# Performance work log

Hardware: AMD Instinct MI355X
Metric: run time of the kernel (lower is better)

## Reference

```python
import jax, jax.numpy as jnp
import numpy as np
from jax import lax

VOL, PATCH, DIM, DEPTH, HEADS, DIM_HEAD, MLP, CH, B = 64, 8, 768, 4, 12, 64, 3072, 1, 2
INNER = HEADS * DIM_HEAD
GS = VOL // PATCH              # 8 -> N = 512 tokens
EPS = 1e-5


def _sincos_1d(embed_dim, pos):
    omega = np.arange(embed_dim // 2, dtype=float) / (embed_dim / 2.0)
    omega = 1.0 / 10000 ** omega
    out = np.einsum('m,d->md', pos.reshape(-1), omega)
    return np.concatenate([np.sin(out), np.cos(out)], axis=1)


def _pos_embed_3d(embed_dim, gs):
    gd = np.arange(gs, dtype=np.float32)
    gh = np.arange(gs, dtype=np.float32)
    gw = np.arange(gs, dtype=np.float32)
    grid = np.stack(np.meshgrid(gw, gh, gd), axis=0).reshape([3, 1, gs, gs, gs])
    emb = np.concatenate([_sincos_1d(embed_dim // 3, grid[i]) for i in range(3)], axis=1)
    return jnp.asarray(emb, jnp.float32)[None]  # [1, N, dim]


def setup_inputs() -> dict:
    key = jax.random.key(0)
    ks = jax.random.split(key, 12)
    s = 0.02  # xavier-like small init scale
    d = {
        'volume': jax.random.normal(ks[0], (B, CH, VOL, VOL, VOL), jnp.float32),
        'conv_w': jax.random.normal(ks[1], (DIM, CH, PATCH, PATCH, PATCH), jnp.float32) * s,
        'conv_b': jnp.zeros((DIM,), jnp.float32),
        'pos_embed': _pos_embed_3d(DIM, GS),
        'ln1_w': jnp.ones((DEPTH, DIM), jnp.float32),
        'ln1_b': jnp.zeros((DEPTH, DIM), jnp.float32),
        'w_qkv': jax.random.normal(ks[2], (DEPTH, DIM, 3 * INNER), jnp.float32) * s,
        'w_o': jax.random.normal(ks[3], (DEPTH, INNER, DIM), jnp.float32) * s,
        'b_o': jnp.zeros((DEPTH, DIM), jnp.float32),
        'ln2_w': jnp.ones((DEPTH, DIM), jnp.float32),
        'ln2_b': jnp.zeros((DEPTH, DIM), jnp.float32),
        'w1': jax.random.normal(ks[4], (DEPTH, DIM, MLP), jnp.float32) * s,
        'b1': jnp.zeros((DEPTH, MLP), jnp.float32),
        'w2': jax.random.normal(ks[5], (DEPTH, MLP, DIM), jnp.float32) * s,
        'b2': jnp.zeros((DEPTH, DIM), jnp.float32),
        'lnf_w': jnp.ones((DIM,), jnp.float32),
        'lnf_b': jnp.zeros((DIM,), jnp.float32),
    }
    return d


def _ln(x, w, b):
    m = jnp.mean(x, axis=-1, keepdims=True)
    v = jnp.mean(jnp.square(x - m), axis=-1, keepdims=True)
    return (x - m) * lax.rsqrt(v + EPS) * w + b


def _forward(volume, conv_w, conv_b, pos_embed, ln1_w, ln1_b, w_qkv, w_o, b_o,
             ln2_w, ln2_b, w1, b1, w2, b2, lnf_w, lnf_b):
    # Conv3d patch embedding (stride == kernel == patch)
    x = lax.conv_general_dilated(volume, conv_w, window_strides=(PATCH,) * 3,
                                 padding='VALID',
                                 dimension_numbers=('NCDHW', 'OIDHW', 'NCDHW'))
    x = x + conv_b[None, :, None, None, None]
    b = x.shape[0]
    x = x.reshape(b, DIM, -1).transpose(0, 2, 1)   # b (d h w) c -> [B, N, dim]
    x = x + pos_embed
    scale = DIM_HEAD ** -0.5

    def layer(x, p):
        l1w, l1b, wqkv, wo, bo, l2w, l2b, W1, B1, W2, B2 = p
        h = _ln(x, l1w, l1b)
        qkv = h @ wqkv                               # [B, N, 3*inner]
        q, k, v = jnp.split(qkv, 3, axis=-1)
        def heads(t):
            bsz, n, _ = t.shape
            return t.reshape(bsz, n, HEADS, DIM_HEAD).transpose(0, 2, 1, 3)
        q, k, v = heads(q), heads(k), heads(v)
        attn = jax.nn.softmax(jnp.einsum('bhqd,bhkd->bhqk', q, k) * scale, axis=-1)
        o = jnp.einsum('bhqk,bhkd->bhqd', attn, v)   # [B, H, N, dh]
        o = o.transpose(0, 2, 1, 3).reshape(x.shape[0], -1, INNER)
        x = x + (o @ wo + bo)
        h = _ln(x, l2w, l2b)
        x = x + (jnp.tanh(h @ W1 + B1) @ W2 + B2)
        return x, None

    params = (ln1_w, ln1_b, w_qkv, w_o, b_o, ln2_w, ln2_b, w1, b1, w2, b2)
    x, _ = lax.scan(layer, x, params)
    return _ln(x, lnf_w, lnf_b)


def reference(volume, conv_w, conv_b, pos_embed, ln1_w, ln1_b, w_qkv, w_o, b_o,
              ln2_w, ln2_b, w1, b1, w2, b2, lnf_w, lnf_b):
    return _forward(volume, conv_w, conv_b, pos_embed, ln1_w, ln1_b, w_qkv, w_o, b_o,
                    ln2_w, ln2_b, w1, b1, w2, b2, lnf_w, lnf_b)
```

## Files before the change

### kernel.cpp

```cpp
#include <hip/hip_runtime.h>
#include <hip/hip_bf16.h>

typedef __hip_bfloat16 bf16;
typedef short bf16x8 __attribute__((ext_vector_type(8)));
typedef float f32x4 __attribute__((ext_vector_type(4)));

__device__ __forceinline__ float b2f(bf16 v) { return __bfloat162float(v); }
__device__ __forceinline__ void storev(float* p, float v) { *p = v; }
__device__ __forceinline__ void storev(bf16* p, float v) { *p = __float2bfloat16(v); }

__device__ __forceinline__ void store4(float* p, float a, float b, float c, float d) {
  *(float4*)p = make_float4(a, b, c, d);
}
__device__ __forceinline__ void store4(bf16* p, float a, float b, float c, float d) {
  bf16 pk[4] = {__float2bfloat16(a), __float2bfloat16(b), __float2bfloat16(c),
                __float2bfloat16(d)};
  *(uint2*)p = *(uint2*)pk;
}

__device__ __forceinline__ void gl2lds16(const bf16* g, bf16* l) {
  __builtin_amdgcn_global_load_lds(
      (const __attribute__((address_space(1))) unsigned int*)g,
      (__attribute__((address_space(3))) unsigned int*)l, 16, 0, 0);
}
__device__ __forceinline__ void gl2lds16f(const float* g, float* l) {
  __builtin_amdgcn_global_load_lds(
      (const __attribute__((address_space(1))) unsigned int*)g,
      (__attribute__((address_space(3))) unsigned int*)l, 16, 0, 0);
}

__global__ __launch_bounds__(256) void prologue_all(
    const float* __restrict__ wqkv, const float* __restrict__ wo,
    const float* __restrict__ w1, const float* __restrict__ w2,
    bf16* __restrict__ tqkv, bf16* __restrict__ two,
    bf16* __restrict__ t1, bf16* __restrict__ t2,
    const float* __restrict__ convw, bf16* __restrict__ cwb,
    const float* __restrict__ vol, bf16* __restrict__ patchA) {
  int bid = blockIdx.x;
  size_t L = blockIdx.y;
  int tid = threadIdx.x;

  if (bid >= 864) {
    if (bid < 960) {
      int cid = (bid - 864) * 4 + (int)L;
      int i = (cid * 256 + tid) * 4;
      float4 v = *(const float4*)&convw[i];
      bf16 pk[4] = {__float2bfloat16(v.x), __float2bfloat16(v.y),
                    __float2bfloat16(v.z), __float2bfloat16(v.w)};
      *(uint2*)&cwb[i] = *(uint2*)pk;
    } else {
      int t = (bid - 960) * 4 + (int)L;
      int b = t >> 9, n = t & 511;
      int pd = n >> 6, ph = (n >> 3) & 7, pw = n & 7;
      const float* vb = vol + ((size_t)b << 18);
      for (int l = tid; l < 512; l += 256) {
        int i = l >> 6, j = (l >> 3) & 7, k = l & 7;
        patchA[(size_t)t * 512 + l] =
            __float2bfloat16(vb[(pd * 8 + i) * 4096 + (ph * 8 + j) * 64 + (pw * 8 + k)]);
      }
    }
    return;
  }

  const float* in;
  bf16* out;
  int R, C, tc, t0;
  if (bid < 216)       { in = wqkv + L * 768 * 2304; out = tqkv + L * 768 * 2304; R = 768;  C = 2304; tc = 36; t0 = bid; }
  else if (bid < 288)  { in = wo + L * 768 * 768;    out = two + L * 768 * 768;   R = 768;  C = 768;  tc = 12; t0 = bid - 216; }
  else if (bid < 576)  { in = w1 + L * 768 * 3072;   out = t1 + L * 768 * 3072;   R = 768;  C = 3072; tc = 48; t0 = bid - 288; }
  else                 { in = w2 + L * 3072 * 768;   out = t2 + L * 3072 * 768;   R = 3072; C = 768;  tc = 12; t0 = bid - 576; }
  int r0 = (t0 / tc) * 128, c0 = (t0 % tc) * 64;
  __shared__ float tile[8192];
#pragma unroll
  for (int it = 0; it < 8; ++it) {
    int s = tid + it * 256;
    int r = s >> 4, cc = s & 15;
    int csrc = (cc ^ ((r >> 3) & 7)) << 2;
    gl2lds16f(&in[(size_t)(r0 + r) * C + c0 + csrc], &tile[s * 4]);
  }
  __syncthreads();
#pragma unroll
  for (int it = 0; it < 4; ++it) {
    int idx = tid + it * 256;
    int c = idx >> 4, rb = (idx & 15) * 8;
    int slot = (c >> 2) ^ ((rb >> 3) & 7);
    int base = rb * 64 + slot * 4 + (c & 3);
    bf16 pk[8];
#pragma unroll
    for (int e = 0; e < 8; ++e) pk[e] = __float2bfloat16(tile[base + e * 64]);
    *(uint4*)&out[(size_t)(c0 + c) * R + r0 + rb] = *(uint4*)pk;
  }
}

template <typename OutT>
__global__ __launch_bounds__(256) void ln_kernel(const float* __restrict__ x,
                                                 const float* __restrict__ w,
                                                 const float* __restrict__ b,
                                                 OutT* __restrict__ out) {
  int row = (blockIdx.x << 2) + (threadIdx.x >> 6);
  int lane = threadIdx.x & 63;
  const float* xr = x + (size_t)row * 768;
  float4 v[3];
  float s = 0.f, ss = 0.f;
#pragma unroll
  for (int j = 0; j < 3; ++j) {
    v[j] = *(const float4*)&xr[j * 256 + lane * 4];
    s += v[j].x + v[j].y + v[j].z + v[j].w;
    ss += v[j].x * v[j].x + v[j].y * v[j].y + v[j].z * v[j].z + v[j].w * v[j].w;
  }
#pragma unroll
  for (int off = 32; off; off >>= 1) {
    s += __shfl_xor(s, off);
    ss += __shfl_xor(ss, off);
  }
  float m = s * (1.f / 768.f);
  float r = rsqrtf(ss * (1.f / 768.f) - m * m + 1e-5f);
  OutT* orow = out + (size_t)row * 768;
#pragma unroll
  for (int j = 0; j < 3; ++j) {
    int cidx = j * 256 + lane * 4;
    float4 wv = *(const float4*)&w[cidx];
    float4 bv = *(const float4*)&b[cidx];
    store4(orow + cidx,
           (v[j].x - m) * r * wv.x + bv.x,
           (v[j].y - m) * r * wv.y + bv.y,
           (v[j].z - m) * r * wv.z + bv.z,
           (v[j].w - m) * r * wv.w + bv.w);
  }
}

template <int BM, int BN, int WR, int WC, int EPI>
__global__ __launch_bounds__(256) void mfma_gemm(
    const bf16* __restrict__ A, const bf16* __restrict__ Bt,
    const float* __restrict__ bias, const float* __restrict__ aux,
    bf16* __restrict__ vt,
    void* __restrict__ Cout, int M, int N, int K) {
  constexpr int WTM = BM / WR, WTN = BN / WC;
  constexpr int MT = WTM / 16, NT = WTN / 16;
  __shared__ bf16 As[BM * 64];
  __shared__ bf16 Bs[BN * 64];
  int tid = threadIdx.x;
  int wave = tid >> 6, lane = tid & 63;
  int wm = wave / WC, wn = wave % WC;
  int m15 = lane & 15, q = lane >> 4;
  int m0 = blockIdx.y * BM, n0 = blockIdx.x * BN;
  int kspan = K / gridDim.z;
  int kbeg = blockIdx.z * kspan, kend = kbeg + kspan;

  f32x4 acc[MT][NT];
#pragma unroll
  for (int i = 0; i < MT; ++i)
#pragma unroll
    for (int j = 0; j < NT; ++j) acc[i][j] = (f32x4){0.f, 0.f, 0.f, 0.f};

  for (int k0 = kbeg; k0 < kend; k0 += 64) {
#pragma unroll
    for (int it = 0; it < BM * 8 / 256; ++it) {
      int c = tid + it * 256;
      int row = c >> 3, cc = c & 7;
      gl2lds16(&A[(size_t)(m0 + row) * K + k0 + cc * 8], &As[c * 8]);
    }
#pragma unroll
    for (int it = 0; it < BN * 8 / 256; ++it) {
      int c = tid + it * 256;
      int row = c >> 3, cc = c & 7;
      gl2lds16(&Bt[(size_t)(n0 + row) * K + k0 + cc * 8], &Bs[c * 8]);
    }
    __syncthreads();
#pragma unroll
    for (int s = 0; s < 2; ++s) {
      bf16x8 af[MT], bfr[NT];
#pragma unroll
      for (int i = 0; i < MT; ++i)
        af[i] = *(const bf16x8*)&As[(wm * WTM + i * 16 + m15) * 64 + s * 32 + q * 8];
#pragma unroll
      for (int j = 0; j < NT; ++j)
        bfr[j] = *(const bf16x8*)&Bs[(wn * WTN + j * 16 + m15) * 64 + s * 32 + q * 8];
#pragma unroll
      for (int i = 0; i < MT; ++i)
#pragma unroll
        for (int j = 0; j < NT; ++j)
          acc[i][j] = __builtin_amdgcn_mfma_f32_16x16x32_bf16(af[i], bfr[j], acc[i][j], 0, 0, 0);
    }
    __syncthreads();
  }

#pragma unroll
  for (int i = 0; i < MT; ++i) {
#pragma unroll
    for (int j = 0; j < NT; ++j) {
      int col = n0 + wn * WTN + j * 16 + m15;
      if (EPI == 4) {
        if (col < 1536) {
#pragma unroll
          for (int r = 0; r < 4; ++r) {
            int row = m0 + wm * WTM + i * 16 + q * 4 + r;
            ((bf16*)Cout)[(size_t)row * 1536 + col] = __float2bfloat16(acc[i][j][r]);
          }
        } else {
          int row0 = m0 + wm * WTM + i * 16 + q * 4;
          int cl = col - 1536;
          int hh = cl >> 6, dd = cl & 63;
          int bb = row0 >> 9, tok = row0 & 511;
          bf16 pk[4];
#pragma unroll
          for (int r = 0; r < 4; ++r) pk[r] = __float2bfloat16(acc[i][j][r]);
          *(uint2*)&vt[((size_t)(bb * 12 + hh) * 64 + dd) * 512 + tok] = *(uint2*)pk;
        }
      } else if (EPI == 5) {
        float bv = (blockIdx.z == 0) ? bias[col] : 0.f;
#pragma unroll
        for (int r = 0; r < 4; ++r) {
          int row = m0 + wm * WTM + i * 16 + q * 4 + r;
          unsafeAtomicAdd(&((float*)Cout)[(size_t)row * N + col], acc[i][j][r] + bv);
        }
      } else {
        float bv = (EPI == 0) ? 0.f : bias[col];
#pragma unroll
        for (int r = 0; r < 4; ++r) {
          int row = m0 + wm * WTM + i * 16 + q * 4 + r;
          float v = acc[i][j][r] + bv;
          if (EPI == 2) v = tanhf(v);
          if (EPI == 3) v += aux[(size_t)(row & 511) * N + col];
          if (EPI == 0 || EPI == 2)
            ((bf16*)Cout)[(size_t)row * N + col] = __float2bfloat16(v);
          else
            ((float*)Cout)[(size_t)row * N + col] = v;
        }
      }
    }
  }
}

__global__ __launch_bounds__(128) void attn_mfma(const bf16* __restrict__ qk,
                                                 const bf16* __restrict__ Vt,
                                                 bf16* __restrict__ o) {
  constexpr int PS = 520;
  __shared__ bf16 KVs[2][64 * 64];
  __shared__ bf16 P[32 * PS];
  int bh = blockIdx.x;
  int b = bh / 12, hh = bh % 12;
  int q0 = blockIdx.y * 32;
  int tid = threadIdx.x;
  int wave = tid >> 6, lane = tid & 63;
  int n15 = lane & 15, quad = lane >> 4;
  const bf16* qkb = qk + (size_t)b * 512 * 1536;
  int ql = wave * 16 + n15;

  const bf16* qp = qkb + (size_t)(q0 + ql) * 1536 + hh * 64 + quad * 8;
  bf16x8 qf0 = *(const bf16x8*)qp;
  bf16x8 qf1 = *(const bf16x8*)(qp + 32);

  f32x4 S[32];
#pragma unroll
  for (int i = 0; i < 32; ++i) S[i] = (f32x4){0.f, 0.f, 0.f, 0.f};

  const bf16* kbase = qkb + 768 + hh * 64;
#pragma unroll
  for (int kr = 0; kr < 4; ++kr) {
    __syncthreads();
#pragma unroll
    for (int h = 0; h < 2; ++h) {
      int kc = kr * 2 + h;
#pragma unroll
      for (int it = 0; it < 4; ++it) {
        int c = tid + it * 128;
        int r = c >> 3, cc = c & 7;
        gl2lds16(&kbase[(size_t)(kc * 64 + r) * 1536 + cc * 8], &KVs[h][c * 8]);
      }
    }
    __syncthreads();
#pragma unroll
    for (int h = 0; h < 2; ++h) {
      int kc = kr * 2 + h;
#pragma unroll
      for (int t = 0; t < 4; ++t) {
        int idx = kc * 4 + t;
        bf16x8 a0 = *(const bf16x8*)&KVs[h][(t * 16 + n15) * 64 + quad * 8];
        bf16x8 a1 = *(const bf16x8*)&KVs[h][(t * 16 + n15) * 64 + 32 + quad * 8];
        S[idx] = __builtin_amdgcn_mfma_f32_16x16x32_bf16(a0, qf0, S[idx], 0, 0, 0);
        S[idx] = __builtin_amdgcn_mfma_f32_16x16x32_bf16(a1, qf1, S[idx], 0, 0, 0);
      }
    }
  }

  float mx = -1e30f;
#pragma unroll
  for (int i = 0; i < 32; ++i)
#pragma unroll
    for (int r = 0; r < 4; ++r) { S[i][r] *= 0.125f; mx = fmaxf(mx, S[i][r]); }
  mx = fmaxf(mx, __shfl_xor(mx, 16));
  mx = fmaxf(mx, __shfl_xor(mx, 32));
  float sum = 0.f;
#pragma unroll
  for (int i = 0; i < 32; ++i)
#pragma unroll
    for (int r = 0; r < 4; ++r) { float e = __expf(S[i][r] - mx); S[i][r] = e; sum += e; }
  sum += __shfl_xor(sum, 16);
  sum += __shfl_xor(sum, 32);
  float inv = 1.f / sum;

#pragma unroll
  for (int i = 0; i < 32; ++i) {
    bf16 pk[4];
#pragma unroll
    for (int r = 0; r < 4; ++r) pk[r] = __float2bfloat16(S[i][r] * inv);
    *(uint2*)&P[(size_t)ql * PS + i * 16 + quad * 4] = *(uint2*)pk;
  }

  f32x4 oacc[4];
#pragma unroll
  for (int dt = 0; dt < 4; ++dt) oacc[dt] = (f32x4){0.f, 0.f, 0.f, 0.f};
  const bf16* vtb = Vt + (size_t)bh * 64 * 512;
#pragma unroll
  for (int kr = 0; kr < 4; ++kr) {
    __syncthreads();
#pragma unroll
    for (int h = 0; h < 2; ++h) {
      int kv = kr * 2 + h;
#pragma unroll
      for (int it = 0; it < 4; ++it) {
        int c = tid + it * 128;
        int r = c >> 3, cc = c & 7;
        gl2lds16(&vtb[(size_t)r * 512 + kv * 64 + cc * 8], &KVs[h][c * 8]);
      }
    }
    __syncthreads();
#pragma unroll
    for (int h = 0; h < 2; ++h) {
      int kv = kr * 2 + h;
      bf16x8 p0 = *(const bf16x8*)&P[(size_t)ql * PS + kv * 64 + quad * 8];
      bf16x8 p1 = *(const bf16x8*)&P[(size_t)ql * PS + kv * 64 + 32 + quad * 8];
#pragma unroll
      for (int dt = 0; dt < 4; ++dt) {
        bf16x8 v0 = *(const bf16x8*)&KVs[h][(dt * 16 + n15) * 64 + quad * 8];
        bf16x8 v1 = *(const bf16x8*)&KVs[h][(dt * 16 + n15) * 64 + 32 + quad * 8];
        oacc[dt] = __builtin_amdgcn_mfma_f32_16x16x32_bf16(p0, v0, oacc[dt], 0, 0, 0);
        oacc[dt] = __builtin_amdgcn_mfma_f32_16x16x32_bf16(p1, v1, oacc[dt], 0, 0, 0);
      }
    }
  }

#pragma unroll
  for (int dt = 0; dt < 4; ++dt)
#pragma unroll
    for (int r = 0; r < 4; ++r) {
      int tok = q0 + wave * 16 + quad * 4 + r;
      o[((size_t)b * 512 + tok) * 768 + hh * 64 + dt * 16 + n15] =
          __float2bfloat16(oacc[dt][r]);
    }
}

extern "C" void kernel_launch(void* const* d_in, const int* in_sizes, int n_in,
                              void* d_out, int out_size, void* d_ws, size_t ws_size,
                              hipStream_t stream) {
  const float* volume = (const float*)d_in[0];
  const float* conv_w = (const float*)d_in[1];
  const float* conv_b = (const float*)d_in[2];
  const float* pos    = (const float*)d_in[3];
  const float* ln1w   = (const float*)d_in[4];
  const float* ln1b   = (const float*)d_in[5];
  const float* wqkv   = (const float*)d_in[6];
  const float* wo     = (const float*)d_in[7];
  const float* bo     = (const float*)d_in[8];
  const float* ln2w   = (const float*)d_in[9];
  const float* ln2b   = (const float*)d_in[10];
  const float* w1     = (const float*)d_in[11];
  const float* b1     = (const float*)d_in[12];
  const float* w2     = (const float*)d_in[13];
  const float* b2     = (const float*)d_in[14];
  const float* lnfw   = (const float*)d_in[15];
  const float* lnfb   = (const float*)d_in[16];

  char* w = (char*)d_ws;
  float* x    = (float*)(w + 0);
  bf16* h     = (bf16*)(w + 3145728);
  bf16* qk    = (bf16*)(w + 4718592);
  bf16* patchA= qk;
  bf16* Vt    = (bf16*)(w + 7864320);
  bf16* oact  = (bf16*)(w + 9437184);
  bf16* cwb   = (bf16*)(w + 15728640);
  bf16* tqkv  = (bf16*)(w + 16515072);
  bf16* two   = (bf16*)(w + 30670848);
  bf16* t1    = (bf16*)(w + 35389440);
  bf16* t2    = (bf16*)(w + 54263808);

  prologue_all<<<dim3(1216, 4), 256, 0, stream>>>(
      wqkv, wo, w1, w2, tqkv, two, t1, t2, conv_w, cwb, volume, patchA);
  mfma_gemm<64, 64, 2, 2, 3><<<dim3(12, 16), 256, 0, stream>>>(
      patchA, cwb, conv_b, pos, nullptr, x, 1024, 768, 512);

  for (int L = 0; L < 4; ++L) {
    ln_kernel<bf16><<<256, 256, 0, stream>>>(x, ln1w + L * 768, ln1b + L * 768, h);
    mfma_gemm<64, 64, 2, 2, 4><<<dim3(36, 16), 256, 0, stream>>>(
        h, tqkv + (size_t)L * 768 * 2304, nullptr, nullptr, Vt, qk, 1024, 2304, 768);
    attn_mfma<<<dim3(24, 16), 128, 0, stream>>>(qk, Vt, oact);
    mfma_gemm<64, 64, 2, 2, 5><<<dim3(12, 16, 2), 256, 0, stream>>>(
        oact, two + (size_t)L * 768 * 768, bo + L * 768, nullptr, nullptr, x, 1024, 768, 768);
    ln_kernel<bf16><<<256, 256, 0, stream>>>(x, ln2w + L * 768, ln2b + L * 768, h);
    mfma_gemm<64, 64, 2, 2, 2><<<dim3(48, 16), 256, 0, stream>>>(
        h, t1 + (size_t)L * 768 * 3072, b1 + L * 3072, nullptr, nullptr, oact, 1024, 3072, 768);
    mfma_gemm<64, 64, 2, 2, 5><<<dim3(12, 16, 4), 256, 0, stream>>>(
        oact, t2 + (size_t)L * 768 * 3072, b2 + L * 768, nullptr, nullptr, x, 1024, 768, 3072);
  }

  ln_kernel<float><<<256, 256, 0, stream>>>(x, lnfw, lnfb, (float*)d_out);
}
```

Before: 497.3 us.

## Switch GEMM to 32x32x16 MFMA with XOR-swizzled LDS layout

Each wave in the 64x64 GEMM tile now computes one 32x32 output block with the 32x32x16 bf16 MFMA instead of four 16x16x32 tiles. LDS chunks are XOR-swizzled by row when loaded from global memory, which is meant to remove bank conflicts on the fragment reads. The goal is fewer LDS fragment loads per MFMA and conflict-free shared-memory access. The epilogues are rewritten for the 32x32 accumulator layout, and the WR/WC template parameters are removed in favour of a hardcoded 2x2 wave grid.

```diff
diff --git a/kernel.cpp b/kernel.cpp
--- a/kernel.cpp
+++ b/kernel.cpp
@@ -4,6 +4,7 @@
 typedef __hip_bfloat16 bf16;
 typedef short bf16x8 __attribute__((ext_vector_type(8)));
 typedef float f32x4 __attribute__((ext_vector_type(4)));
+typedef float f32x16 __attribute__((ext_vector_type(16)));
 
 __device__ __forceinline__ float b2f(bf16 v) { return __bfloat162float(v); }
 __device__ __forceinline__ void storev(float* p, float v) { *p = v; }
@@ -129,105 +130,95 @@
   }
 }
 
-template <int BM, int BN, int WR, int WC, int EPI>
+template <int BM, int BN, int EPI>
 __global__ __launch_bounds__(256) void mfma_gemm(
     const bf16* __restrict__ A, const bf16* __restrict__ Bt,
     const float* __restrict__ bias, const float* __restrict__ aux,
     bf16* __restrict__ vt,
     void* __restrict__ Cout, int M, int N, int K) {
-  constexpr int WTM = BM / WR, WTN = BN / WC;
-  constexpr int MT = WTM / 16, NT = WTN / 16;
   __shared__ bf16 As[BM * 64];
   __shared__ bf16 Bs[BN * 64];
   int tid = threadIdx.x;
   int wave = tid >> 6, lane = tid & 63;
-  int wm = wave / WC, wn = wave % WC;
-  int m15 = lane & 15, q = lane >> 4;
+  int wm = wave >> 1, wn = wave & 1;
+  int l31 = lane & 31, half = lane >> 5;
   int m0 = blockIdx.y * BM, n0 = blockIdx.x * BN;
   int kspan = K / gridDim.z;
   int kbeg = blockIdx.z * kspan, kend = kbeg + kspan;
 
-  f32x4 acc[MT][NT];
-#pragma unroll
-  for (int i = 0; i < MT; ++i)
-#pragma unroll
-    for (int j = 0; j < NT; ++j) acc[i][j] = (f32x4){0.f, 0.f, 0.f, 0.f};
+  f32x16 acc;
+#pragma unroll
+  for (int r = 0; r < 16; ++r) acc[r] = 0.f;
+
+  int arow = wm * 32 + l31;
+  int brow = wn * 32 + l31;
+  int axor = arow & 7, bxor = brow & 7;
 
   for (int k0 = kbeg; k0 < kend; k0 += 64) {
 #pragma unroll
     for (int it = 0; it < BM * 8 / 256; ++it) {
       int c = tid + it * 256;
       int row = c >> 3, cc = c & 7;
-      gl2lds16(&A[(size_t)(m0 + row) * K + k0 + cc * 8], &As[c * 8]);
+      gl2lds16(&A[(size_t)(m0 + row) * K + k0 + (cc ^ (row & 7)) * 8], &As[c * 8]);
     }
 #pragma unroll
     for (int it = 0; it < BN * 8 / 256; ++it) {
       int c = tid + it * 256;
       int row = c >> 3, cc = c & 7;
-      gl2lds16(&Bt[(size_t)(n0 + row) * K + k0 + cc * 8], &Bs[c * 8]);
-    }
-    __syncthreads();
-#pragma unroll
-    for (int s = 0; s < 2; ++s) {
-      bf16x8 af[MT], bfr[NT];
-#pragma unroll
-      for (int i = 0; i < MT; ++i)
-        af[i] = *(const bf16x8*)&As[(wm * WTM + i * 16 + m15) * 64 + s * 32 + q * 8];
-#pragma unroll
-      for (int j = 0; j < NT; ++j)
-        bfr[j] = *(const bf16x8*)&Bs[(wn * WTN + j * 16 + m15) * 64 + s * 32 + q * 8];
-#pragma unroll
-      for (int i = 0; i < MT; ++i)
-#pragma unroll
-        for (int j = 0; j < NT; ++j)
-          acc[i][j] = __builtin_amdgcn_mfma_f32_16x16x32_bf16(af[i], bfr[j], acc[i][j], 0, 0, 0);
-    }
-    __syncthreads();
-  }
-
-#pragma unroll
-  for (int i = 0; i < MT; ++i) {
-#pragma unroll
-    for (int j = 0; j < NT; ++j) {
-      int col = n0 + wn * WTN + j * 16 + m15;
-      if (EPI == 4) {
-        if (col < 1536) {
-#pragma unroll
-          for (int r = 0; r < 4; ++r) {
-            int row = m0 + wm * WTM + i * 16 + q * 4 + r;
-            ((bf16*)Cout)[(size_t)row * 1536 + col] = __float2bfloat16(acc[i][j][r]);
-          }
-        } else {
-          int row0 = m0 + wm * WTM + i * 16 + q * 4;
-          int cl = col - 1536;
-          int hh = cl >> 6, dd = cl & 63;
-          int bb = row0 >> 9, tok = row0 & 511;
-          bf16 pk[4];
-#pragma unroll
-          for (int r = 0; r < 4; ++r) pk[r] = __float2bfloat16(acc[i][j][r]);
-          *(uint2*)&vt[((size_t)(bb * 12 + hh) * 64 + dd) * 512 + tok] = *(uint2*)pk;
-        }
-      } else if (EPI == 5) {
-        float bv = (blockIdx.z == 0) ? bias[col] : 0.f;
-#pragma unroll
-        for (int r = 0; r < 4; ++r) {
-          int row = m0 + wm * WTM + i * 16 + q * 4 + r;
-          unsafeAtomicAdd(&((float*)Cout)[(size_t)row * N + col], acc[i][j][r] + bv);
-        }
-      } else {
-        float bv = (EPI == 0) ? 0.f : bias[col];
-#pragma unroll
-        for (int r = 0; r < 4; ++r) {
-          int row = m0 + wm * WTM + i * 16 + q * 4 + r;
-          float v = acc[i][j][r] + bv;
-          if (EPI == 2) v = tanhf(v);
-          if (EPI == 3) v += aux[(size_t)(row & 511) * N + col];
-          if (EPI == 0 || EPI == 2)
-            ((bf16*)Cout)[(size_t)row * N + col] = __float2bfloat16(v);
-          else
-            ((float*)Cout)[(size_t)row * N + col] = v;
-        }
-      }
+      gl2lds16(&Bt[(size_t)(n0 + row) * K + k0 + (cc ^ (row & 7)) * 8], &Bs[c * 8]);
+    }
+    __syncthreads();
+#pragma unroll
+    for (int kk = 0; kk < 4; ++kk) {
+      int j = kk * 2 + half;
+      bf16x8 af = *(const bf16x8*)&As[arow * 64 + (j ^ axor) * 8];
+      bf16x8 bfr = *(const bf16x8*)&Bs[brow * 64 + (j ^ bxor) * 8];
+      acc = __builtin_amdgcn_mfma_f32_32x32x16_bf16(af, bfr, acc, 0, 0, 0);
+    }
+    __syncthreads();
+  }
+
+  int col = n0 + wn * 32 + l31;
+  int rbase = m0 + wm * 32 + 4 * half;
+  if (EPI == 4) {
+    if (col < 1536) {
+#pragma unroll
+      for (int r = 0; r < 16; ++r) {
+        int row = rbase + (r & 3) + 8 * (r >> 2);
+        ((bf16*)Cout)[(size_t)row * 1536 + col] = __float2bfloat16(acc[r]);
+      }
+    } else {
+      int cl = col - 1536;
+      int hh = cl >> 6, dd = cl & 63;
+#pragma unroll
+      for (int g = 0; g < 4; ++g) {
+        int row0 = rbase + 8 * g;
+        int bb = row0 >> 9, tok = row0 & 511;
+        bf16 pk[4];
+#pragma unroll
+        for (int t = 0; t < 4; ++t) pk[t] = __float2bfloat16(acc[g * 4 + t]);
+        *(uint2*)&vt[((size_t)(bb * 12 + hh) * 64 + dd) * 512 + tok] = *(uint2*)pk;
+      }
+    }
+  } else if (EPI == 5) {
+    float bv = (blockIdx.z == 0) ? bias[col] : 0.f;
+#pragma unroll
+    for (int r = 0; r < 16; ++r) {
+      int row = rbase + (r & 3) + 8 * (r >> 2);
+      unsafeAtomicAdd(&((float*)Cout)[(size_t)row * N + col], acc[r] + bv);
+    }
+  } else {
+    float bv = (EPI == 0) ? 0.f : bias[col];
+#pragma unroll
+    for (int r = 0; r < 16; ++r) {
+      int row = rbase + (r & 3) + 8 * (r >> 2);
+      float v = acc[r] + bv;
+      if (EPI == 2) v = tanhf(v);
+      if (EPI == 3) v += aux[(size_t)(row & 511) * N + col];
+      if (EPI == 0 || EPI == 2)
+        ((bf16*)Cout)[(size_t)row * N + col] = __float2bfloat16(v);
+      else
+        ((float*)Cout)[(size_t)row * N + col] = v;
     }
   }
 }
@@ -387,20 +378,20 @@
 
   prologue_all<<<dim3(1216, 4), 256, 0, stream>>>(
       wqkv, wo, w1, w2, tqkv, two, t1, t2, conv_w, cwb, volume, patchA);
-  mfma_gemm<64, 64, 2, 2, 3><<<dim3(12, 16), 256, 0, stream>>>(
+  mfma_gemm<64, 64, 3><<<dim3(12, 16), 256, 0, stream>>>(
       patchA, cwb, conv_b, pos, nullptr, x, 1024, 768, 512);
 
   for (int L = 0; L < 4; ++L) {
     ln_kernel<bf16><<<256, 256, 0, stream>>>(x, ln1w + L * 768, ln1b + L * 768, h);
-    mfma_gemm<64, 64, 2, 2, 4><<<dim3(36, 16), 256, 0, stream>>>(
+    mfma_gemm<64, 64, 4><<<dim3(36, 16), 256, 0, stream>>>(
         h, tqkv + (size_t)L * 768 * 2304, nullptr, nullptr, Vt, qk, 1024, 2304, 768);
     attn_mfma<<<dim3(24, 16), 128, 0, stream>>>(qk, Vt, oact);
-    mfma_gemm<64, 64, 2, 2, 5><<<dim3(12, 16, 2), 256, 0, stream>>>(
+    mfma_gemm<64, 64, 5><<<dim3(12, 16, 2), 256, 0, stream>>>(
         oact, two + (size_t)L * 768 * 768, bo + L * 768, nullptr, nullptr, x, 1024, 768, 768);
     ln_kernel<bf16><<<256, 256, 0, stream>>>(x, ln2w + L * 768, ln2b + L * 768, h);
-    mfma_gemm<64, 64, 2, 2, 2><<<dim3(48, 16), 256, 0, stream>>>(
+    mfma_gemm<64, 64, 2><<<dim3(48, 16), 256, 0, stream>>>(
         h, t1 + (size_t)L * 768 * 3072, b1 + L * 3072, nullptr, nullptr, oact, 1024, 3072, 768);
-    mfma_gemm<64, 64, 2, 2, 5><<<dim3(12, 16, 4), 256, 0, stream>>>(
+    mfma_gemm<64, 64, 5><<<dim3(12, 16, 4), 256, 0, stream>>>(
         oact, t2 + (size_t)L * 768 * 3072, b2 + L * 768, nullptr, nullptr, x, 1024, 768, 3072);
   }
 
```

After: 470.0 us (median of 2 runs). 5.5% less time.
